# Kernel tuning notes

Hardware: AMD Instinct MI355X
Metric: run time of the kernel (lower is better)

Reference implementation:

```python
import jax, jax.numpy as jnp
import numpy as np

ROUTINGS = 3


def squash(v):
    # squash along last axis: v/|v| * |v|^2/(1+|v|^2)
    norm = jnp.linalg.norm(v, axis=-1, keepdims=True)
    ns = norm * norm
    return v / norm * (ns / (1.0 + ns))


def setup_inputs() -> dict:
    key = jax.random.key(0)
    k1, k2 = jax.random.split(key)
    B, N, I, D, Din = 256, 10, 1152, 16, 8
    inputs = jax.random.normal(k1, (B, I, Din), dtype=jnp.float32)
    # glorot-uniform-ish init for W [N, I, D, Din]
    limit = np.sqrt(6.0 / (D + Din)).astype(np.float32)
    W = jax.random.uniform(k2, (N, I, D, Din), dtype=jnp.float32,
                           minval=-limit, maxval=limit)
    return {"inputs": inputs, "W": W}


def reference(inputs, W):
    # inputs: [B, I, Din], W: [N, I, D, Din]
    # u_hat[b,n,i,d] = sum_k W[n,i,d,k] * inputs[b,i,k]  (replaces tf.map_fn)
    u_hat = jnp.einsum('nidk,bik->bnid', W, inputs)  # [B, N, I, D]
    b = jnp.zeros(u_hat.shape[:3], dtype=u_hat.dtype)  # [B, N, I]
    outputs = None
    for r in range(ROUTINGS):
        c = jax.nn.softmax(b, axis=1)  # softmax over output capsules N
        outputs = squash(jnp.einsum('bni,bnid->bnd', c, u_hat))  # [B, N, D]
        if r < ROUTINGS - 1:
            # agreement: a[b,n,i] = <outputs[b,n,:], u_hat[b,n,i,:]>
            b = b + jnp.einsum('bnd,bnid->bni', outputs, u_hat)
    return outputs
```

## Files before the change

### kernel.cpp

```cpp
#include <hip/hip_runtime.h>
#include <hip/hip_bf16.h>
#include <stdint.h>


#define BN 256
#define NN 10
#define II 1152
#define DD 16
#define KK 8
#define NT 18
#define NP 5
#define NCH 3
#define CHI 384

typedef unsigned short ushort_t;
typedef unsigned int uint_t;

__device__ __forceinline__ float bflo(uint_t u) {
    union { uint_t i; float f; } v; v.i = u << 16; return v.f;
}
__device__ __forceinline__ float bfhi(uint_t u) {
    union { uint_t i; float f; } v; v.i = u & 0xffff0000u; return v.f;
}
__device__ __forceinline__ uint_t pkbf(float lo, float hi) {
    __hip_bfloat162 h = __float22bfloat162_rn(make_float2(lo, hi));
    uint_t u; __builtin_memcpy(&u, &h, sizeof(u)); return u;
}

__global__ __launch_bounds__(256) void caps_uhat_s0(const float* __restrict__ xg,
                                                    const float* __restrict__ wg,
                                                    ushort_t* __restrict__ u,
                                                    float* __restrict__ part0,
                                                    int b0, int c4)
{
    __shared__ float wlds[4][2048];
    __shared__ float redn[4][64][2];
    const int tid = threadIdx.x;
    const int lane = tid & 63, wv = tid >> 6;
    const int dq = lane & 3, il = lane >> 2;
    const int nb8 = gridDim.x >> 3;
    const int L   = (blockIdx.x & 7) * nb8 + (blockIdx.x >> 3);
    const int it  = L / (NP * c4);
    const int rem = L - it * (NP * c4);
    const int np  = rem / c4;
    const int bl  = (rem - np * c4) * 4;
    const int n0  = np * 2;
    const int i = it * 64 + wv * 16 + il;

    const bool h0 = (il & 1), h1 = (il >> 1) & 1, h2 = (il >> 2) & 1, h3 = (il >> 3) & 1;
    float* myred = &redn[wv][lane][0];
    float* mylds = &wlds[wv][0];
    const int lrow = lane >> 5, lc = lane & 31;
    const float4* wtile0 = (const float4*)(wg + (size_t)(n0 * II + it * 64 + wv * 16) * (DD * KK));

#define STAGE_W(NNV)                                                         \
    {                                                                        \
        const float4* wt = wtile0 + (size_t)(NNV) * II * 32;                 \
        _Pragma("unroll")                                                    \
        for (int j = 0; j < 8; ++j) {                                        \
            int row = lrow + 2 * j;                                          \
            int chunk = row * 32 + (lc ^ (row & 7));                         \
            __builtin_amdgcn_global_load_lds(                                \
                (const __attribute__((address_space(1))) void*)(wt + chunk), \
                (__attribute__((address_space(3))) void*)(mylds + j * 256),  \
                16, 0, 0);                                                   \
        }                                                                    \
    }

    STAGE_W(0);

    float xv[4][8];
#pragma unroll
    for (int bb = 0; bb < 4; ++bb) {
        const float4* xp = (const float4*)(xg + ((size_t)(b0 + bl + bb) * II + i) * KK);
        float4 x0 = xp[0], x1 = xp[1];
        xv[bb][0] = x0.x; xv[bb][1] = x0.y; xv[bb][2] = x0.z; xv[bb][3] = x0.w;
        xv[bb][4] = x1.x; xv[bb][5] = x1.y; xv[bb][6] = x1.z; xv[bb][7] = x1.w;
    }

    auto compute_n = [&](int n, const float4* w, int slot) {
        float s[4][4];
#pragma unroll
        for (int dj = 0; dj < 4; ++dj) {
            float4 wa = w[2 * dj], wb = w[2 * dj + 1];
#pragma unroll
            for (int bb = 0; bb < 4; ++bb) {
                s[bb][dj] = wa.x * xv[bb][0] + wa.y * xv[bb][1]
                          + wa.z * xv[bb][2] + wa.w * xv[bb][3]
                          + wb.x * xv[bb][4] + wb.y * xv[bb][5]
                          + wb.z * xv[bb][6] + wb.w * xv[bb][7];
            }
        }
#pragma unroll
        for (int bb = 0; bb < 4; ++bb) {
            uint2 q;
            q.x = pkbf(s[bb][0], s[bb][1]);
            q.y = pkbf(s[bb][2], s[bb][3]);
            *(uint2*)(u + (((size_t)(bl + bb) * NN + n) * II + i) * DD + dq * 4) = q;
        }
        float v8[8];
#pragma unroll
        for (int k = 0; k < 8; ++k) {
            float a0 = s[(2 * k) >> 2][(2 * k) & 3];
            float a1 = s[(2 * k + 1) >> 2][(2 * k + 1) & 3];
            float give = h0 ? a0 : a1;
            float got  = __shfl_xor(give, 4, 64);
            v8[k] = (h0 ? a1 : a0) + got;
        }
        float v4[4];
#pragma unroll
        for (int k = 0; k < 4; ++k) {
            float a0 = v8[2 * k], a1 = v8[2 * k + 1];
            float give = h1 ? a0 : a1;
            float got  = __shfl_xor(give, 8, 64);
            v4[k] = (h1 ? a1 : a0) + got;
        }
        float v2[2];
#pragma unroll
        for (int k = 0; k < 2; ++k) {
            float a0 = v4[2 * k], a1 = v4[2 * k + 1];
            float give = h2 ? a0 : a1;
            float got  = __shfl_xor(give, 16, 64);
            v2[k] = (h2 ? a1 : a0) + got;
        }
        {
            float a0 = v2[0], a1 = v2[1];
            float give = h3 ? a0 : a1;
            float got  = __shfl_xor(give, 32, 64);
            myred[slot] = (h3 ? a1 : a0) + got;
        }
    };

    float4 w[8];
    asm volatile("s_waitcnt vmcnt(0)" ::: "memory");
#pragma unroll
    for (int jj = 0; jj < 8; ++jj)
        w[jj] = *(const float4*)(mylds + il * 128 + dq * 32 + ((jj ^ (il & 7)) << 2));
    asm volatile("s_waitcnt lgkmcnt(0)" ::: "memory");
    STAGE_W(1);
    compute_n(n0, w, 0);

    asm volatile("s_waitcnt vmcnt(0)" ::: "memory");
#pragma unroll
    for (int jj = 0; jj < 8; ++jj)
        w[jj] = *(const float4*)(mylds + il * 128 + dq * 32 + ((jj ^ (il & 7)) << 2));
    compute_n(n0 + 1, w, 1);
#undef STAGE_W

    __syncthreads();
    if (tid < 128) {
        int bb = tid >> 5, r5 = tid & 31, nn = r5 >> 4, d = r5 & 15;
        int lane2 = ((bb * 4 + (d & 3)) << 2) + (d >> 2);
        float v = redn[0][lane2][nn] + redn[1][lane2][nn]
                + redn[2][lane2][nn] + redn[3][lane2][nn];
        part0[((size_t)(b0 + bl + bb) * NT + it) * 160 + (n0 + nn) * 16 + d] = 0.1f * v;
    }
}

__device__ __forceinline__ void block_reduce_part(float sp[NN][4], int tid,
                                                  float* red,
                                                  float* __restrict__ partp)
{
#pragma unroll
    for (int m = 4; m <= 32; m <<= 1)
#pragma unroll
        for (int n = 0; n < NN; ++n)
#pragma unroll
            for (int j = 0; j < 4; ++j)
                sp[n][j] += __shfl_xor(sp[n][j], m, 64);

    const int lane = tid & 63, wv = tid >> 6, ld = tid & 3;
    if (lane < 4) {
#pragma unroll
        for (int n = 0; n < NN; ++n)
#pragma unroll
            for (int j = 0; j < 4; ++j)
                red[(wv * NN + n) * 16 + ld * 4 + j] = sp[n][j];
    }
    __syncthreads();
    if (tid < 160) {
        int n = tid >> 4, dd = tid & 15;
        float v = 0.f;
#pragma unroll
        for (int w = 0; w < 4; ++w) v += red[(w * NN + n) * 16 + dd];
        partp[tid] = v;
    }
}

__global__ __launch_bounds__(256) void caps_sweep(const ushort_t* __restrict__ u,
                                                  const float* __restrict__ p0,
                                                  const float* __restrict__ p1,
                                                  float* __restrict__ pout, int b0)
{
    __shared__ float red[4 * 160];
    __shared__ float o_s[160];
    const int tid = threadIdx.x, g = tid >> 2, ld = tid & 3;
    const int cb = blockIdx.x / NCH, ch = blockIdx.x % NCH;
    const int b = b0 + cb;
    const ushort_t* ub = u + (size_t)cb * (NN * II * DD);

    const int i0 = ch * CHI + g;
    uint2 r[NN];
#pragma unroll
    for (int n = 0; n < NN; ++n)
        r[n] = *(const uint2*)(ub + ((size_t)(n * II + i0)) * DD + ld * 4);

    if (tid < 160) {
        float v = 0.f;
#pragma unroll
        for (int t = 0; t < NT; ++t)
            v += p0[((size_t)b * NT + t) * 160 + tid];
        float sq = v * v;
#pragma unroll
        for (int m = 1; m <= 8; m <<= 1) sq += __shfl_xor(sq, m, 64);
        float o = v * (sqrtf(sq) / (1.0f + sq));
        if (p1) {
            float v1 = 0.f;
#pragma unroll
            for (int c2 = 0; c2 < NCH; ++c2)
                v1 += p1[((size_t)b * NCH + c2) * 160 + tid];
            float sq1 = v1 * v1;
#pragma unroll
            for (int m = 1; m <= 8; m <<= 1) sq1 += __shfl_xor(sq1, m, 64);
            o += v1 * (sqrtf(sq1) / (1.0f + sq1));
        }
        o_s[tid] = o;
    }
    __syncthreads();

    float sp[NN][4];
#pragma unroll
    for (int n = 0; n < NN; ++n)
#pragma unroll
        for (int j = 0; j < 4; ++j) sp[n][j] = 0.f;

#pragma unroll
    for (int step = 0; step < CHI / 64; ++step) {
        uint2 rn[NN];
        if (step + 1 < CHI / 64) {
            const int i2 = i0 + (step + 1) * 64;
#pragma unroll
            for (int n = 0; n < NN; ++n)
                rn[n] = *(const uint2*)(ub + ((size_t)(n * II + i2)) * DD + ld * 4);
        }

        float p[NN];
#pragma unroll
        for (int n = 0; n < NN; ++n) {
            float4 o4 = *(const float4*)&o_s[(n << 4) + (ld << 2)];
            p[n] = bflo(r[n].x) * o4.x + bfhi(r[n].x) * o4.y
                 + bflo(r[n].y) * o4.z + bfhi(r[n].y) * o4.w;
        }
        float a[NN];
#pragma unroll
        for (int n = 0; n < NN; ++n) {
            float t2 = p[n] + __shfl_xor(p[n], 1, 64);
            a[n] = t2 + __shfl_xor(t2, 2, 64);
        }
        float m = a[0];
#pragma unroll
        for (int n = 1; n < NN; ++n) m = fmaxf(m, a[n]);
        float c[NN], ssum = 0.f;
#pragma unroll
        for (int n = 0; n < NN; ++n) { c[n] = __expf(a[n] - m); ssum += c[n]; }
        float inv = 1.0f / ssum;
#pragma unroll
        for (int n = 0; n < NN; ++n) {
            float w = c[n] * inv;
            sp[n][0] += w * bflo(r[n].x); sp[n][1] += w * bfhi(r[n].x);
            sp[n][2] += w * bflo(r[n].y); sp[n][3] += w * bfhi(r[n].y);
        }
        if (step + 1 < CHI / 64) {
#pragma unroll
            for (int n = 0; n < NN; ++n) r[n] = rn[n];
        }
    }
    block_reduce_part(sp, tid, red, pout + ((size_t)b * NCH + ch) * 160);
}

__global__ __launch_bounds__(192) void caps_out(const float* __restrict__ p2,
                                                float* __restrict__ out, int b0)
{
    const int b = b0 + blockIdx.x;
    const int t = threadIdx.x;
    if (t < 160) {
        float v = 0.f;
#pragma unroll
        for (int ch = 0; ch < NCH; ++ch)
            v += p2[((size_t)b * NCH + ch) * 160 + t];
        float sq = v * v;
#pragma unroll
        for (int m = 1; m <= 8; m <<= 1) sq += __shfl_xor(sq, m, 64);
        out[(size_t)b * 160 + t] = v * (sqrtf(sq) / (1.0f + sq));
    }
}

extern "C" void kernel_launch(void* const* d_in, const int* in_sizes, int n_in,
                              void* d_out, int out_size, void* d_ws, size_t ws_size,
                              hipStream_t stream)
{
    const float* xg = (const float*)d_in[0];
    const float* wg = (const float*)d_in[1];
    if (n_in >= 2 && in_sizes[0] == NN * II * DD * KK) {
        const float* t = xg; xg = wg; wg = t;
    }
    float* outp = (float*)d_out;

    const size_t perB  = (size_t)NN * II * DD * 2;
    const size_t p0B   = (size_t)BN * NT * 160 * 4;
    const size_t p12B  = (size_t)BN * NCH * 160 * 4;
    size_t extra = p0B + 2 * p12B;
    size_t avail = (ws_size > extra) ? ws_size - extra : 0;
    int C = 256;
    if (avail < (size_t)256 * perB) {
        C = (int)(avail / perB);
        C &= ~15;
        if (C < 16) C = 16;
    }
    ushort_t* uws = (ushort_t*)d_ws;
    float* part0 = (float*)((char*)d_ws + (size_t)C * perB);
    float* part1 = part0 + (size_t)BN * NT * 160;
    float* part2 = part1 + (size_t)BN * NCH * 160;

    for (int b0 = 0; b0 < BN; b0 += C) {
        int c = (BN - b0 < C) ? (BN - b0) : C;
        int c4 = c / 4;
        caps_uhat_s0<<<NT * NP * c4, 256, 0, stream>>>(xg, wg, uws, part0, b0, c4);
        caps_sweep  <<<c * NCH, 256, 0, stream>>>(uws, part0, nullptr, part1, b0);
        caps_sweep  <<<c * NCH, 256, 0, stream>>>(uws, part0, part1,  part2, b0);
        caps_out    <<<c,       192, 0, stream>>>(part2, outp, b0);
    }
}
```

Before: 141.3 us.

## Triple-buffer u_hat loads in routing sweep and rework W LDS swizzle

The routing sweep kernel now keeps three register buffers of u_hat, issuing loads two steps ahead instead of one so more global-load latency is hidden behind compute. The softmax max and sum reductions are rebalanced into trees to shorten dependency chains. Separately, the W tile swizzle in the projection kernel is changed to a smaller XOR pattern, with reads rotated per lane quad to cut LDS bank conflicts. The extra prefetch buffer raises VGPR pressure, which may reduce occupancy.

```diff
diff --git a/kernel.cpp b/kernel.cpp
--- a/kernel.cpp
+++ b/kernel.cpp
@@ -51,6 +51,7 @@
     float* myred = &redn[wv][lane][0];
     float* mylds = &wlds[wv][0];
     const int lrow = lane >> 5, lc = lane & 31;
+    const int gsw = (il & 3) << 1;
     const float4* wtile0 = (const float4*)(wg + (size_t)(n0 * II + it * 64 + wv * 16) * (DD * KK));
 
 #define STAGE_W(NNV)                                                         \
@@ -59,7 +60,7 @@
         _Pragma("unroll")                                                    \
         for (int j = 0; j < 8; ++j) {                                        \
             int row = lrow + 2 * j;                                          \
-            int chunk = row * 32 + (lc ^ (row & 7));                         \
+            int chunk = row * 32 + (lc ^ ((row & 3) << 1));                  \
             __builtin_amdgcn_global_load_lds(                                \
                 (const __attribute__((address_space(1))) void*)(wt + chunk), \
                 (__attribute__((address_space(3))) void*)(mylds + j * 256),  \
@@ -134,16 +135,16 @@
     float4 w[8];
     asm volatile("s_waitcnt vmcnt(0)" ::: "memory");
 #pragma unroll
-    for (int jj = 0; jj < 8; ++jj)
-        w[jj] = *(const float4*)(mylds + il * 128 + dq * 32 + ((jj ^ (il & 7)) << 2));
+    for (int m = 0; m < 8; ++m)
+        w[m ^ dq] = *(const float4*)(mylds + il * 128 + (((dq * 8 + (m ^ dq)) ^ gsw) << 2));
     asm volatile("s_waitcnt lgkmcnt(0)" ::: "memory");
     STAGE_W(1);
     compute_n(n0, w, 0);
 
     asm volatile("s_waitcnt vmcnt(0)" ::: "memory");
 #pragma unroll
-    for (int jj = 0; jj < 8; ++jj)
-        w[jj] = *(const float4*)(mylds + il * 128 + dq * 32 + ((jj ^ (il & 7)) << 2));
+    for (int m = 0; m < 8; ++m)
+        w[m ^ dq] = *(const float4*)(mylds + il * 128 + (((dq * 8 + (m ^ dq)) ^ gsw) << 2));
     compute_n(n0 + 1, w, 1);
 #undef STAGE_W
 
@@ -198,12 +199,16 @@
     const int cb = blockIdx.x / NCH, ch = blockIdx.x % NCH;
     const int b = b0 + cb;
     const ushort_t* ub = u + (size_t)cb * (NN * II * DD);
-
     const int i0 = ch * CHI + g;
-    uint2 r[NN];
-#pragma unroll
-    for (int n = 0; n < NN; ++n)
-        r[n] = *(const uint2*)(ub + ((size_t)(n * II + i0)) * DD + ld * 4);
+
+#define ULOAD(R, S)                                                            \
+    _Pragma("unroll")                                                          \
+    for (int n = 0; n < NN; ++n)                                               \
+        R[n] = *(const uint2*)(ub + ((size_t)(n * II + i0 + (S) * 64)) * DD + ld * 4);
+
+    uint2 rA[NN], rB[NN], rC[NN];
+    ULOAD(rA, 0)
+    ULOAD(rB, 1)
 
     if (tid < 160) {
         float v = 0.f;
@@ -234,47 +239,49 @@
 #pragma unroll
         for (int j = 0; j < 4; ++j) sp[n][j] = 0.f;
 
-#pragma unroll
-    for (int step = 0; step < CHI / 64; ++step) {
-        uint2 rn[NN];
-        if (step + 1 < CHI / 64) {
-            const int i2 = i0 + (step + 1) * 64;
-#pragma unroll
-            for (int n = 0; n < NN; ++n)
-                rn[n] = *(const uint2*)(ub + ((size_t)(n * II + i2)) * DD + ld * 4);
-        }
-
-        float p[NN];
-#pragma unroll
-        for (int n = 0; n < NN; ++n) {
-            float4 o4 = *(const float4*)&o_s[(n << 4) + (ld << 2)];
-            p[n] = bflo(r[n].x) * o4.x + bfhi(r[n].x) * o4.y
-                 + bflo(r[n].y) * o4.z + bfhi(r[n].y) * o4.w;
-        }
-        float a[NN];
-#pragma unroll
-        for (int n = 0; n < NN; ++n) {
-            float t2 = p[n] + __shfl_xor(p[n], 1, 64);
-            a[n] = t2 + __shfl_xor(t2, 2, 64);
-        }
-        float m = a[0];
-#pragma unroll
-        for (int n = 1; n < NN; ++n) m = fmaxf(m, a[n]);
-        float c[NN], ssum = 0.f;
-#pragma unroll
-        for (int n = 0; n < NN; ++n) { c[n] = __expf(a[n] - m); ssum += c[n]; }
-        float inv = 1.0f / ssum;
-#pragma unroll
-        for (int n = 0; n < NN; ++n) {
-            float w = c[n] * inv;
-            sp[n][0] += w * bflo(r[n].x); sp[n][1] += w * bfhi(r[n].x);
-            sp[n][2] += w * bflo(r[n].y); sp[n][3] += w * bfhi(r[n].y);
-        }
-        if (step + 1 < CHI / 64) {
-#pragma unroll
-            for (int n = 0; n < NN; ++n) r[n] = rn[n];
-        }
-    }
+#define STEP(R)                                                                \
+    {                                                                          \
+        float p[NN];                                                           \
+        _Pragma("unroll")                                                      \
+        for (int n = 0; n < NN; ++n) {                                         \
+            float4 o4 = *(const float4*)&o_s[(n << 4) + (ld << 2)];            \
+            p[n] = bflo(R[n].x) * o4.x + bfhi(R[n].x) * o4.y                   \
+                 + bflo(R[n].y) * o4.z + bfhi(R[n].y) * o4.w;                  \
+        }                                                                      \
+        float a[NN];                                                           \
+        _Pragma("unroll")                                                      \
+        for (int n = 0; n < NN; ++n) {                                         \
+            float t2 = p[n] + __shfl_xor(p[n], 1, 64);                         \
+            a[n] = t2 + __shfl_xor(t2, 2, 64);                                 \
+        }                                                                      \
+        float m01 = fmaxf(fmaxf(a[0], a[1]), a[2]);                            \
+        float m2  = fmaxf(fmaxf(a[3], a[4]), a[5]);                            \
+        float m3  = fmaxf(fmaxf(a[6], a[7]), a[8]);                            \
+        float mx  = fmaxf(fmaxf(m01, m2), fmaxf(m3, a[9]));                    \
+        float c[NN];                                                           \
+        _Pragma("unroll")                                                      \
+        for (int n = 0; n < NN; ++n) c[n] = __expf(a[n] - mx);                 \
+        float s01 = c[0] + c[1], s23 = c[2] + c[3], s45 = c[4] + c[5];         \
+        float s67 = c[6] + c[7], s89 = c[8] + c[9];                            \
+        float ssum = ((s01 + s23) + (s45 + s67)) + s89;                        \
+        float inv = 1.0f / ssum;                                               \
+        _Pragma("unroll")                                                      \
+        for (int n = 0; n < NN; ++n) {                                         \
+            float w = c[n] * inv;                                              \
+            sp[n][0] += w * bflo(R[n].x); sp[n][1] += w * bfhi(R[n].x);        \
+            sp[n][2] += w * bflo(R[n].y); sp[n][3] += w * bfhi(R[n].y);        \
+        }                                                                      \
+    }
+
+    ULOAD(rC, 2)  STEP(rA)
+    ULOAD(rA, 3)  STEP(rB)
+    ULOAD(rB, 4)  STEP(rC)
+    ULOAD(rC, 5)  STEP(rA)
+    STEP(rB)
+    STEP(rC)
+#undef ULOAD
+#undef STEP
+
     block_reduce_part(sp, tid, red, pout + ((size_t)b * NCH + ch) * 160);
 }
 
```

Result: slower. 301.6 us (+113.4%).
